# Kernel tuning notes

Hardware: AMD Instinct MI355X
Metric: run time of the kernel (lower is better)

The kernel has to match this reference:

```python
import jax, jax.numpy as jnp
import numpy as np

NUM_HEADS = 16
HEAD_DIM = 128


def apply_rope(x, rope):
    # x: [B, H, N, D]; rope: [N, 1, D]
    freqs = rope[:, 0, :]  # [N, D]
    cos = jnp.repeat(freqs[:, 0::2], 2, axis=-1)[None, None]  # [1,1,N,D]
    sin = jnp.repeat(freqs[:, 1::2], 2, axis=-1)[None, None]
    xr = x.reshape(*x.shape[:-1], -1, 2)
    x_real, x_imag = xr[..., 0], xr[..., 1]
    x_rot = jnp.stack([-x_imag, x_real], axis=-1).reshape(x.shape)
    return (x * cos + x_rot * sin).astype(x.dtype)


def setup_inputs() -> dict:
    key = jax.random.key(0)
    k1, k2, k3, k4 = jax.random.split(key, 4)
    B, N, hidden = 2, 2048, 2048
    x = jax.random.normal(k1, (B, N, hidden), dtype=jnp.float32)
    rope = jax.random.uniform(k2, (N, 1, HEAD_DIM), dtype=jnp.float32)
    qkv_w = jax.random.normal(k3, (hidden, 3 * NUM_HEADS * HEAD_DIM), dtype=jnp.float32) * 0.02
    out_w = jax.random.normal(k4, (NUM_HEADS * HEAD_DIM, hidden), dtype=jnp.float32) * 0.02
    return {"x": x, "rope": rope, "qkv_w": qkv_w, "out_w": out_w}


def reference(x, rope, qkv_w, out_w):
    B, N, _ = x.shape
    H, D = NUM_HEADS, HEAD_DIM
    qkv = (x @ qkv_w).reshape(B, N, 3, H, D)  # [B,N,3,H,D]
    q = jnp.transpose(qkv[:, :, 0], (0, 2, 1, 3))  # [B,H,N,D]
    k = jnp.transpose(qkv[:, :, 1], (0, 2, 1, 3))
    v = jnp.transpose(qkv[:, :, 2], (0, 2, 1, 3))
    q = apply_rope(q, rope)
    k = apply_rope(k, rope)
    scale = 1.0 / np.float32(np.sqrt(D))
    scores = jnp.einsum('bhqd,bhkd->bhqk', q, k) * scale
    attn = jax.nn.softmax(scores, axis=-1)
    out = jnp.einsum('bhqk,bhkd->bhqd', attn, v)
    out = jnp.transpose(out, (0, 2, 1, 3)).reshape(B, N, H * D)
    return out @ out_w
```

## Files before the change

### kernel.cpp

```cpp
#include <hip/hip_runtime.h>
#include <stdint.h>


typedef unsigned short u16;
typedef __bf16 bf16x8 __attribute__((ext_vector_type(8)));
typedef float f32x4 __attribute__((ext_vector_type(4)));

#define DI static __device__ __forceinline__

DI u16 f2b(float f) {
  union { float f; unsigned u; } v; v.f = f;
  unsigned r = v.u + 0x7FFFu + ((v.u >> 16) & 1u);
  return (u16)(r >> 16);
}

typedef unsigned int __attribute__((address_space(1))) *gas1_t;
typedef unsigned int __attribute__((address_space(3))) *las3_t;

DI void async16(const void* g, void* l) {
  __builtin_amdgcn_global_load_lds((gas1_t)g, (las3_t)l, 16, 0, 0);
}

DI bf16x8 ldsv(const u16* p) { return *(const bf16x8*)p; }

__global__ void k_cvt(const float* __restrict__ in, u16* __restrict__ out, int n4) {
  int i = blockIdx.x * blockDim.x + threadIdx.x;
  if (i >= n4) return;
  float4 v = ((const float4*)in)[i];
  ushort4 o;
  o.x = f2b(v.x); o.y = f2b(v.y); o.z = f2b(v.z); o.w = f2b(v.w);
  ((ushort4*)out)[i] = o;
}

__global__ void k_tcvt(const float* __restrict__ in, u16* __restrict__ out, int R, int C) {
  __shared__ float t[32][33];
  int bx = blockIdx.x * 32, by = blockIdx.y * 32;
  int tx = threadIdx.x, ty = threadIdx.y;
#pragma unroll
  for (int i = 0; i < 4; i++)
    t[ty + i * 8][tx] = in[(size_t)(by + ty + i * 8) * C + bx + tx];
  __syncthreads();
#pragma unroll
  for (int i = 0; i < 4; i++)
    out[(size_t)(bx + ty + i * 8) * R + by + tx] = f2b(t[tx][ty + i * 8]);
}

template <int MODE>
__global__ __launch_bounds__(256) void k_gemm(
    const u16* __restrict__ A, const u16* __restrict__ BT, const int K,
    float* __restrict__ C, const int ldc,
    const float* __restrict__ rope,
    u16* __restrict__ Qp, u16* __restrict__ Kp, u16* __restrict__ VTp) {
  __shared__ u16 As[4096];
  __shared__ u16 Bs[4096];
  const int tid = threadIdx.x;
  const int w = tid >> 6, lane = tid & 63;
  const int g = lane >> 4, lr = lane & 15;
  const int wm = (w >> 1) << 6, wn = (w & 1) << 6;
  const int bm0 = blockIdx.y << 7, bn0 = blockIdx.x << 7;

  const int cg = (lane & 3) ^ ((lane >> 3) & 3);
  const int l4 = lane >> 2;
  const int gsw = g ^ ((lr >> 1) & 3);

  const u16* Ag = A + (size_t)(bm0 + (w << 5) + l4) * K + (cg << 3);
  const u16* Bg = BT + (size_t)(bn0 + (w << 5) + l4) * K + (cg << 3);
  u16* Asd = As + (w << 10);
  u16* Bsd = Bs + (w << 10);
  const size_t rstep = (size_t)K << 4;

  const f32x4 zf = {0.f, 0.f, 0.f, 0.f};
  f32x4 acc[4][4];
#pragma unroll
  for (int i = 0; i < 4; i++)
#pragma unroll
    for (int j = 0; j < 4; j++) acc[i][j] = zf;

  for (int kt = 0; kt < K; kt += 32) {
    async16(Ag + kt, Asd);
    async16(Ag + rstep + kt, Asd + 512);
    async16(Bg + kt, Bsd);
    async16(Bg + rstep + kt, Bsd + 512);
    __syncthreads();
    bf16x8 af[4], bf[4];
#pragma unroll
    for (int i = 0; i < 4; i++) {
      af[i] = ldsv(As + ((wm + (i << 4) + lr) << 5) + (gsw << 3));
      bf[i] = ldsv(Bs + ((wn + (i << 4) + lr) << 5) + (gsw << 3));
    }
#pragma unroll
    for (int i = 0; i < 4; i++)
#pragma unroll
      for (int j = 0; j < 4; j++)
        acc[i][j] = __builtin_amdgcn_mfma_f32_16x16x32_bf16(af[i], bf[j], acc[i][j], 0, 0, 0);
    __syncthreads();
  }

  if constexpr (MODE == 0) {
#pragma unroll
    for (int i = 0; i < 4; i++) {
      const int row0 = bm0 + wm + (i << 4) + (g << 2);
#pragma unroll
      for (int j = 0; j < 4; j++) {
        const int col = bn0 + wn + (j << 4) + lr;
#pragma unroll
        for (int e = 0; e < 4; e++)
          C[(size_t)(row0 + e) * ldc + col] = acc[i][j][e];
      }
    }
  } else {
    const int sidx = bn0 >> 11;
    const int h = (bn0 >> 7) & 15;
    const int b = bm0 >> 11;
    const int nb = (bm0 & 2047) + wm;
    if (sidx < 2) {
      u16* dst = (sidx == 0 ? Qp : Kp) + ((size_t)(b * 16 + h) << 18);
      const float qs = (sidx == 0) ? 0.08838834764831845f : 1.0f;
#pragma unroll
      for (int i = 0; i < 4; i++) {
#pragma unroll
        for (int j = 0; j < 4; j++) {
          const int d = wn + (j << 4) + lr;
          const float sg = (d & 1) ? 1.f : -1.f;
          const int dpe = d & ~1, dpo = d | 1;
#pragma unroll
          for (int e = 0; e < 4; e++) {
            const int n = nb + (i << 4) + (g << 2) + e;
            const float v = acc[i][j][e];
            const float p = __shfl_xor(v, 1);
            const float cf = rope[(n << 7) + dpe];
            const float sf = rope[(n << 7) + dpo];
            dst[((size_t)n << 7) + d] = f2b((v * cf + sg * p * sf) * qs);
          }
        }
      }
    } else {
      u16* dst = VTp + ((size_t)(b * 16 + h) << 18);
#pragma unroll
      for (int i = 0; i < 4; i++) {
#pragma unroll
        for (int j = 0; j < 4; j++) {
          const int d = wn + (j << 4) + lr;
          const int n0 = nb + (i << 4) + (g << 2);
          ushort4 o;
          o.x = f2b(acc[i][j][0]); o.y = f2b(acc[i][j][1]);
          o.z = f2b(acc[i][j][2]); o.w = f2b(acc[i][j][3]);
          *(ushort4*)(dst + ((size_t)d << 11) + n0) = o;
        }
      }
    }
  }
}

__global__ __launch_bounds__(256) void k_attn(
    const u16* __restrict__ Q, const u16* __restrict__ Kt,
    const u16* __restrict__ VT, u16* __restrict__ Og) {
  __shared__ u16 KV[16384];
  __shared__ u16 Pb[4][4096];
  const int tid = threadIdx.x;
  const int w = tid >> 6, lane = tid & 63;
  const int g = lane >> 4, lr = lane & 15;
  const int qt = blockIdx.x, h = blockIdx.y, b = blockIdx.z;
  const size_t bh = (size_t)(b * 16 + h) << 18;
  const u16* Qb = Q + bh;
  const u16* Kb = Kt + bh;
  const u16* Vb = VT + bh;
  u16* Pw = &Pb[w][0];

  const int qr0 = (qt << 7) + (w << 5);
  bf16x8 qf[2][4];
#pragma unroll
  for (int mi = 0; mi < 2; mi++)
#pragma unroll
    for (int kk = 0; kk < 4; kk++)
      qf[mi][kk] = *(const bf16x8*)(Qb + ((size_t)(qr0 + (mi << 4) + lr) << 7) + (kk << 5) + (g << 3));

  const f32x4 zf = {0.f, 0.f, 0.f, 0.f};
  f32x4 o[2][8];
  float m_[2][4], l_[2][4];
#pragma unroll
  for (int mi = 0; mi < 2; mi++) {
#pragma unroll
    for (int ni = 0; ni < 8; ni++) o[mi][ni] = zf;
#pragma unroll
    for (int e = 0; e < 4; e++) { m_[mi][e] = -3.0e38f; l_[mi][e] = 0.f; }
  }

  for (int kt = 0; kt < 16; kt++) {
#pragma unroll
    for (int q = 0; q < 8; q++) {
      const int r = (((w << 3) + q) << 2) + g;
      const int cc = lr ^ (((q << 2) + g) & 7);
      async16(Kb + ((size_t)((kt << 7) + r) << 7) + (cc << 3), KV + (((w << 3) + q) << 9));
    }
    __syncthreads();
    f32x4 s[2][8];
#pragma unroll
    for (int mi = 0; mi < 2; mi++)
#pragma unroll
      for (int ni = 0; ni < 8; ni++) s[mi][ni] = zf;
#pragma unroll
    for (int kk = 0; kk < 4; kk++) {
      bf16x8 kf[8];
#pragma unroll
      for (int ni = 0; ni < 8; ni++) {
        const int row = (ni << 4) + lr;
        kf[ni] = ldsv(KV + (row << 7) + ((((kk << 2) + g) ^ (row & 7)) << 3));
      }
#pragma unroll
      for (int mi = 0; mi < 2; mi++)
#pragma unroll
        for (int ni = 0; ni < 8; ni++)
          s[mi][ni] = __builtin_amdgcn_mfma_f32_16x16x32_bf16(qf[mi][kk], kf[ni], s[mi][ni], 0, 0, 0);
    }
    __syncthreads();
#pragma unroll
    for (int q = 0; q < 8; q++) {
      const int r = (((w << 3) + q) << 2) + g;
      const int cc = lr ^ (((q << 2) + g) & 7);
      async16(Vb + ((size_t)r << 11) + (kt << 7) + (cc << 3), KV + (((w << 3) + q) << 9));
    }
#pragma unroll
    for (int mi = 0; mi < 2; mi++) {
      float mx[4], al[4], ps[4];
#pragma unroll
      for (int e = 0; e < 4; e++) {
        float v = s[mi][0][e];
#pragma unroll
        for (int ni = 1; ni < 8; ni++) v = fmaxf(v, s[mi][ni][e]);
        v = fmaxf(v, __shfl_xor(v, 1));
        v = fmaxf(v, __shfl_xor(v, 2));
        v = fmaxf(v, __shfl_xor(v, 4));
        v = fmaxf(v, __shfl_xor(v, 8));
        mx[e] = fmaxf(v, m_[mi][e]);
        al[e] = __expf(m_[mi][e] - mx[e]);
        m_[mi][e] = mx[e];
        ps[e] = 0.f;
      }
#pragma unroll
      for (int ni = 0; ni < 8; ni++)
#pragma unroll
        for (int e = 0; e < 4; e++) {
          const float p = __expf(s[mi][ni][e] - mx[e]);
          s[mi][ni][e] = p;
          ps[e] += p;
        }
#pragma unroll
      for (int e = 0; e < 4; e++) {
        ps[e] += __shfl_xor(ps[e], 1);
        ps[e] += __shfl_xor(ps[e], 2);
        ps[e] += __shfl_xor(ps[e], 4);
        ps[e] += __shfl_xor(ps[e], 8);
        l_[mi][e] = l_[mi][e] * al[e] + ps[e];
      }
#pragma unroll
      for (int ni = 0; ni < 8; ni++)
#pragma unroll
        for (int e = 0; e < 4; e++) o[mi][ni][e] *= al[e];
#pragma unroll
      for (int ni = 0; ni < 8; ni++)
#pragma unroll
        for (int e = 0; e < 4; e++) {
          const int row = (mi << 4) + (g << 2) + e;
          const int col = (ni << 4) + lr;
          Pw[(row << 7) + (((col >> 3) ^ (row & 7)) << 3) + (col & 7)] = f2b(s[mi][ni][e]);
        }
    }
    __syncthreads();
#pragma unroll
    for (int kk = 0; kk < 4; kk++) {
      bf16x8 pf[2];
#pragma unroll
      for (int mi = 0; mi < 2; mi++) {
        const int row = (mi << 4) + lr;
        pf[mi] = ldsv(Pw + (row << 7) + ((((kk << 2) + g) ^ (row & 7)) << 3));
      }
      bf16x8 vf[8];
#pragma unroll
      for (int ni = 0; ni < 8; ni++) {
        const int d = (ni << 4) + lr;
        vf[ni] = ldsv(KV + (d << 7) + ((((kk << 2) + g) ^ (d & 7)) << 3));
      }
#pragma unroll
      for (int mi = 0; mi < 2; mi++)
#pragma unroll
        for (int ni = 0; ni < 8; ni++)
          o[mi][ni] = __builtin_amdgcn_mfma_f32_16x16x32_bf16(pf[mi], vf[ni], o[mi][ni], 0, 0, 0);
    }
    __syncthreads();
  }
  u16* Ob = Og + ((size_t)b << 22) + (h << 7);
#pragma unroll
  for (int mi = 0; mi < 2; mi++) {
    float inv[4];
#pragma unroll
    for (int e = 0; e < 4; e++) inv[e] = 1.0f / l_[mi][e];
#pragma unroll
    for (int ni = 0; ni < 8; ni++) {
      const int d = (ni << 4) + lr;
#pragma unroll
      for (int e = 0; e < 4; e++) {
        const int n = qr0 + (mi << 4) + (g << 2) + e;
        Ob[((size_t)n << 11) + d] = f2b(o[mi][ni][e] * inv[e]);
      }
    }
  }
}

extern "C" void kernel_launch(void* const* d_in, const int* in_sizes, int n_in,
                              void* d_out, int out_size, void* d_ws, size_t ws_size,
                              hipStream_t stream) {
  const float* x = (const float*)d_in[0];
  const float* rope = (const float*)d_in[1];
  const float* qkv_w = (const float*)d_in[2];
  const float* out_w = (const float*)d_in[3];
  float* out = (float*)d_out;

  char* ws = (char*)d_ws;
  u16* xb    = (u16*)(ws);
  u16* wqkvT = (u16*)(ws + 16777216);
  u16* woT   = (u16*)(ws + 41943040);
  u16* Qp    = (u16*)(ws + 50331648);
  u16* Kp    = (u16*)(ws + 67108864);
  u16* VTp   = (u16*)(ws + 83886080);
  u16* Og    = xb;

  k_cvt<<<8192, 256, 0, stream>>>(x, xb, 2097152);
  k_tcvt<<<dim3(192, 64), dim3(32, 8), 0, stream>>>(qkv_w, wqkvT, 2048, 6144);
  k_tcvt<<<dim3(64, 64), dim3(32, 8), 0, stream>>>(out_w, woT, 2048, 2048);
  k_gemm<1><<<dim3(48, 32), 256, 0, stream>>>(xb, wqkvT, 2048, nullptr, 0, rope, Qp, Kp, VTp);
  k_attn<<<dim3(16, 16, 2), 256, 0, stream>>>(Qp, Kp, VTp, Og);
  k_gemm<0><<<dim3(16, 32), 256, 0, stream>>>(Og, woT, 2048, out, 2048, nullptr, nullptr, nullptr, nullptr);
}
```

Measured before the change: 514.4 us.

## Rework attention pipeline with split K/V buffers, lazy rescale, exp2, deeper GEMM k-tile

The GEMM k-step grows from 32 to 64 with an 8-way XOR swizzle, which halves the number of barrier-separated iterations. Attention now uses 64-key tiles with separate K and V LDS buffers, so the next K/V loads are issued behind the current compute. It also folds log2(e) into the Q scale so it can use exp2, skips output rescaling unless the running max grows by more than 8, adds setprio around MFMA bursts, sets launch bounds to allow 2 blocks per CU, and remaps blocks through a 1D grid. The lazy rescale trades a little numeric headroom for fewer multiplies, and the smaller tile means twice as many loop iterations.

Measured after the change: 442.0 us. 1.16x faster.

```diff
diff --git a/kernel.cpp b/kernel.cpp
--- a/kernel.cpp
+++ b/kernel.cpp
@@ -13,6 +13,12 @@
   unsigned r = v.u + 0x7FFFu + ((v.u >> 16) & 1u);
   return (u16)(r >> 16);
 }
+
+#if __has_builtin(__builtin_amdgcn_exp2f)
+DI float EXP2(float x) { return __builtin_amdgcn_exp2f(x); }
+#else
+DI float EXP2(float x) { return exp2f(x); }
+#endif
 
 typedef unsigned int __attribute__((address_space(1))) *gas1_t;
 typedef unsigned int __attribute__((address_space(3))) *las3_t;
@@ -51,23 +57,22 @@
     float* __restrict__ C, const int ldc,
     const float* __restrict__ rope,
     u16* __restrict__ Qp, u16* __restrict__ Kp, u16* __restrict__ VTp) {
-  __shared__ u16 As[4096];
-  __shared__ u16 Bs[4096];
+  __shared__ u16 As[8192];
+  __shared__ u16 Bs[8192];
   const int tid = threadIdx.x;
   const int w = tid >> 6, lane = tid & 63;
   const int g = lane >> 4, lr = lane & 15;
   const int wm = (w >> 1) << 6, wn = (w & 1) << 6;
   const int bm0 = blockIdx.y << 7, bn0 = blockIdx.x << 7;
 
-  const int cg = (lane & 3) ^ ((lane >> 3) & 3);
-  const int l4 = lane >> 2;
-  const int gsw = g ^ ((lr >> 1) & 3);
-
-  const u16* Ag = A + (size_t)(bm0 + (w << 5) + l4) * K + (cg << 3);
-  const u16* Bg = BT + (size_t)(bn0 + (w << 5) + l4) * K + (cg << 3);
-  u16* Asd = As + (w << 10);
-  u16* Bsd = Bs + (w << 10);
-  const size_t rstep = (size_t)K << 4;
+  const int cg8 = (lane & 7) ^ (lane >> 3);
+  const int row_l = lane >> 3;
+
+  const u16* Ag = A + (size_t)(bm0 + (w << 5) + row_l) * K + (cg8 << 3);
+  const u16* Bg = BT + (size_t)(bn0 + (w << 5) + row_l) * K + (cg8 << 3);
+  u16* Asd = As + (w << 11);
+  u16* Bsd = Bs + (w << 11);
+  const size_t rstep = (size_t)K << 3;
 
   const f32x4 zf = {0.f, 0.f, 0.f, 0.f};
   f32x4 acc[4][4];
@@ -76,23 +81,28 @@
 #pragma unroll
     for (int j = 0; j < 4; j++) acc[i][j] = zf;
 
-  for (int kt = 0; kt < K; kt += 32) {
-    async16(Ag + kt, Asd);
-    async16(Ag + rstep + kt, Asd + 512);
-    async16(Bg + kt, Bsd);
-    async16(Bg + rstep + kt, Bsd + 512);
+  for (int kt = 0; kt < K; kt += 64) {
+#pragma unroll
+    for (int i = 0; i < 4; i++) {
+      async16(Ag + (size_t)i * rstep + kt, Asd + (i << 9));
+      async16(Bg + (size_t)i * rstep + kt, Bsd + (i << 9));
+    }
     __syncthreads();
-    bf16x8 af[4], bf[4];
-#pragma unroll
-    for (int i = 0; i < 4; i++) {
-      af[i] = ldsv(As + ((wm + (i << 4) + lr) << 5) + (gsw << 3));
-      bf[i] = ldsv(Bs + ((wn + (i << 4) + lr) << 5) + (gsw << 3));
-    }
-#pragma unroll
-    for (int i = 0; i < 4; i++)
-#pragma unroll
-      for (int j = 0; j < 4; j++)
-        acc[i][j] = __builtin_amdgcn_mfma_f32_16x16x32_bf16(af[i], bf[j], acc[i][j], 0, 0, 0);
+#pragma unroll
+    for (int kk = 0; kk < 2; kk++) {
+      bf16x8 af[4], bf[4];
+      const int swz = ((((kk << 2) + g) ^ (lr & 7)) << 3);
+#pragma unroll
+      for (int i = 0; i < 4; i++) {
+        af[i] = ldsv(As + ((wm + (i << 4) + lr) << 6) + swz);
+        bf[i] = ldsv(Bs + ((wn + (i << 4) + lr) << 6) + swz);
+      }
+#pragma unroll
+      for (int i = 0; i < 4; i++)
+#pragma unroll
+        for (int j = 0; j < 4; j++)
+          acc[i][j] = __builtin_amdgcn_mfma_f32_16x16x32_bf16(af[i], bf[j], acc[i][j], 0, 0, 0);
+    }
     __syncthreads();
   }
 
@@ -115,7 +125,7 @@
     const int nb = (bm0 & 2047) + wm;
     if (sidx < 2) {
       u16* dst = (sidx == 0 ? Qp : Kp) + ((size_t)(b * 16 + h) << 18);
-      const float qs = (sidx == 0) ? 0.08838834764831845f : 1.0f;
+      const float qs = (sidx == 0) ? 0.08838834764831845f * 1.4426950408889634f : 1.0f;
 #pragma unroll
       for (int i = 0; i < 4; i++) {
 #pragma unroll
@@ -152,15 +162,17 @@
   }
 }
 
-__global__ __launch_bounds__(256) void k_attn(
+__global__ __launch_bounds__(256, 2) void k_attn(
     const u16* __restrict__ Q, const u16* __restrict__ Kt,
     const u16* __restrict__ VT, u16* __restrict__ Og) {
-  __shared__ u16 KV[16384];
-  __shared__ u16 Pb[4][4096];
+  __shared__ u16 Ks[8192];
+  __shared__ u16 Vs[8192];
+  __shared__ u16 Pb[4][2048];
   const int tid = threadIdx.x;
   const int w = tid >> 6, lane = tid & 63;
   const int g = lane >> 4, lr = lane & 15;
-  const int qt = blockIdx.x, h = blockIdx.y, b = blockIdx.z;
+  const int wgid = ((blockIdx.x & 7) << 6) + (blockIdx.x >> 3);
+  const int qt = wgid & 15, h = (wgid >> 4) & 15, b = wgid >> 8;
   const size_t bh = (size_t)(b * 16 + h) << 18;
   const u16* Qb = Q + bh;
   const u16* Kb = Kt + bh;
@@ -175,6 +187,30 @@
     for (int kk = 0; kk < 4; kk++)
       qf[mi][kk] = *(const bf16x8*)(Qb + ((size_t)(qr0 + (mi << 4) + lr) << 7) + (kk << 5) + (g << 3));
 
+  const int krow_l = lane >> 4;
+  const int kcg_base = lane & 15;
+  const int vrow_l = lane >> 3;
+  const int vcg_base = lane & 7;
+
+  auto stageK = [&](int kt) {
+#pragma unroll
+    for (int i = 0; i < 4; i++) {
+      const int grp = (w << 2) + i;
+      const int row = (grp << 2) + krow_l;
+      const int cg = kcg_base ^ (row & 7);
+      async16(Kb + ((size_t)((kt << 6) + row) << 7) + (cg << 3), Ks + (grp << 9));
+    }
+  };
+  auto stageV = [&](int kt) {
+#pragma unroll
+    for (int i = 0; i < 4; i++) {
+      const int grp = (w << 2) + i;
+      const int d = (grp << 3) + vrow_l;
+      const int cg = vcg_base ^ (d & 7);
+      async16(Vb + ((size_t)d << 11) + (kt << 6) + (cg << 3), Vs + (grp << 9));
+    }
+  };
+
   const f32x4 zf = {0.f, 0.f, 0.f, 0.f};
   f32x4 o[2][8];
   float m_[2][4], l_[2][4];
@@ -183,112 +219,139 @@
 #pragma unroll
     for (int ni = 0; ni < 8; ni++) o[mi][ni] = zf;
 #pragma unroll
-    for (int e = 0; e < 4; e++) { m_[mi][e] = -3.0e38f; l_[mi][e] = 0.f; }
-  }
-
-  for (int kt = 0; kt < 16; kt++) {
-#pragma unroll
-    for (int q = 0; q < 8; q++) {
-      const int r = (((w << 3) + q) << 2) + g;
-      const int cc = lr ^ (((q << 2) + g) & 7);
-      async16(Kb + ((size_t)((kt << 7) + r) << 7) + (cc << 3), KV + (((w << 3) + q) << 9));
-    }
-    __syncthreads();
-    f32x4 s[2][8];
-#pragma unroll
-    for (int mi = 0; mi < 2; mi++)
-#pragma unroll
-      for (int ni = 0; ni < 8; ni++) s[mi][ni] = zf;
+    for (int e = 0; e < 4; e++) { m_[mi][e] = -1.0e30f; l_[mi][e] = 0.f; }
+  }
+
+  stageK(0);
+  stageV(0);
+  __syncthreads();
+
+  for (int kt = 0; kt < 32; kt++) {
+    f32x4 s[2][4];
+#pragma unroll
+    for (int mi = 0; mi < 2; mi++)
+#pragma unroll
+      for (int ni = 0; ni < 4; ni++) s[mi][ni] = zf;
 #pragma unroll
     for (int kk = 0; kk < 4; kk++) {
-      bf16x8 kf[8];
-#pragma unroll
-      for (int ni = 0; ni < 8; ni++) {
+      bf16x8 kf[4];
+#pragma unroll
+      for (int ni = 0; ni < 4; ni++) {
         const int row = (ni << 4) + lr;
-        kf[ni] = ldsv(KV + (row << 7) + ((((kk << 2) + g) ^ (row & 7)) << 3));
-      }
+        kf[ni] = ldsv(Ks + (row << 7) + ((((kk << 2) + g) ^ (row & 7)) << 3));
+      }
+      __builtin_amdgcn_s_setprio(1);
 #pragma unroll
       for (int mi = 0; mi < 2; mi++)
 #pragma unroll
-        for (int ni = 0; ni < 8; ni++)
+        for (int ni = 0; ni < 4; ni++)
           s[mi][ni] = __builtin_amdgcn_mfma_f32_16x16x32_bf16(qf[mi][kk], kf[ni], s[mi][ni], 0, 0, 0);
-    }
-    __syncthreads();
-#pragma unroll
-    for (int q = 0; q < 8; q++) {
-      const int r = (((w << 3) + q) << 2) + g;
-      const int cc = lr ^ (((q << 2) + g) & 7);
-      async16(Vb + ((size_t)r << 11) + (kt << 7) + (cc << 3), KV + (((w << 3) + q) << 9));
-    }
-#pragma unroll
-    for (int mi = 0; mi < 2; mi++) {
-      float mx[4], al[4], ps[4];
+      __builtin_amdgcn_s_setprio(0);
+    }
+
+    float pm[2][4];
+#pragma unroll
+    for (int mi = 0; mi < 2; mi++)
 #pragma unroll
       for (int e = 0; e < 4; e++) {
-        float v = s[mi][0][e];
-#pragma unroll
-        for (int ni = 1; ni < 8; ni++) v = fmaxf(v, s[mi][ni][e]);
+        float v = fmaxf(fmaxf(s[mi][0][e], s[mi][1][e]), fmaxf(s[mi][2][e], s[mi][3][e]));
         v = fmaxf(v, __shfl_xor(v, 1));
         v = fmaxf(v, __shfl_xor(v, 2));
         v = fmaxf(v, __shfl_xor(v, 4));
         v = fmaxf(v, __shfl_xor(v, 8));
-        mx[e] = fmaxf(v, m_[mi][e]);
-        al[e] = __expf(m_[mi][e] - mx[e]);
-        m_[mi][e] = mx[e];
-        ps[e] = 0.f;
-      }
-#pragma unroll
-      for (int ni = 0; ni < 8; ni++)
+        pm[mi][e] = v;
+      }
+    bool need = false;
+#pragma unroll
+    for (int mi = 0; mi < 2; mi++)
+#pragma unroll
+      for (int e = 0; e < 4; e++) need = need || (pm[mi][e] > m_[mi][e] + 8.0f);
+    if (__any(need)) {
+      float al[2][4];
+#pragma unroll
+      for (int mi = 0; mi < 2; mi++)
 #pragma unroll
         for (int e = 0; e < 4; e++) {
-          const float p = __expf(s[mi][ni][e] - mx[e]);
+          const float mn = fmaxf(m_[mi][e], pm[mi][e]);
+          const float a = EXP2(m_[mi][e] - mn);
+          m_[mi][e] = mn;
+          l_[mi][e] *= a;
+          al[mi][e] = a;
+        }
+#pragma unroll
+      for (int mi = 0; mi < 2; mi++)
+#pragma unroll
+        for (int ni = 0; ni < 8; ni++)
+#pragma unroll
+          for (int e = 0; e < 4; e++) o[mi][ni][e] *= al[mi][e];
+    }
+    float ps[2][4];
+#pragma unroll
+    for (int mi = 0; mi < 2; mi++)
+#pragma unroll
+      for (int e = 0; e < 4; e++) ps[mi][e] = 0.f;
+#pragma unroll
+    for (int mi = 0; mi < 2; mi++)
+#pragma unroll
+      for (int ni = 0; ni < 4; ni++)
+#pragma unroll
+        for (int e = 0; e < 4; e++) {
+          const float p = EXP2(s[mi][ni][e] - m_[mi][e]);
           s[mi][ni][e] = p;
-          ps[e] += p;
-        }
+          ps[mi][e] += p;
+        }
+#pragma unroll
+    for (int mi = 0; mi < 2; mi++)
 #pragma unroll
       for (int e = 0; e < 4; e++) {
-        ps[e] += __shfl_xor(ps[e], 1);
-        ps[e] += __shfl_xor(ps[e], 2);
-        ps[e] += __shfl_xor(ps[e], 4);
-        ps[e] += __shfl_xor(ps[e], 8);
-        l_[mi][e] = l_[mi][e] * al[e] + ps[e];
-      }
-#pragma unroll
-      for (int ni = 0; ni < 8; ni++)
-#pragma unroll
-        for (int e = 0; e < 4; e++) o[mi][ni][e] *= al[e];
-#pragma unroll
-      for (int ni = 0; ni < 8; ni++)
+        float t = ps[mi][e];
+        t += __shfl_xor(t, 1);
+        t += __shfl_xor(t, 2);
+        t += __shfl_xor(t, 4);
+        t += __shfl_xor(t, 8);
+        l_[mi][e] += t;
+      }
+#pragma unroll
+    for (int mi = 0; mi < 2; mi++)
+#pragma unroll
+      for (int ni = 0; ni < 4; ni++)
 #pragma unroll
         for (int e = 0; e < 4; e++) {
           const int row = (mi << 4) + (g << 2) + e;
           const int col = (ni << 4) + lr;
-          Pw[(row << 7) + (((col >> 3) ^ (row & 7)) << 3) + (col & 7)] = f2b(s[mi][ni][e]);
-        }
-    }
+          Pw[(row << 6) + (((col >> 3) ^ (row & 7)) << 3) + (col & 7)] = f2b(s[mi][ni][e]);
+        }
+
     __syncthreads();
-#pragma unroll
-    for (int kk = 0; kk < 4; kk++) {
+    if (kt < 31) stageK(kt + 1);
+
+#pragma unroll
+    for (int kk = 0; kk < 2; kk++) {
       bf16x8 pf[2];
 #pragma unroll
       for (int mi = 0; mi < 2; mi++) {
         const int row = (mi << 4) + lr;
-        pf[mi] = ldsv(Pw + (row << 7) + ((((kk << 2) + g) ^ (row & 7)) << 3));
+        pf[mi] = ldsv(Pw + (row << 6) + ((((kk << 2) + g) ^ (row & 7)) << 3));
       }
       bf16x8 vf[8];
 #pragma unroll
       for (int ni = 0; ni < 8; ni++) {
         const int d = (ni << 4) + lr;
-        vf[ni] = ldsv(KV + (d << 7) + ((((kk << 2) + g) ^ (d & 7)) << 3));
-      }
+        vf[ni] = ldsv(Vs + (d << 6) + ((((kk << 2) + g) ^ (d & 7)) << 3));
+      }
+      __builtin_amdgcn_s_setprio(1);
 #pragma unroll
       for (int mi = 0; mi < 2; mi++)
 #pragma unroll
         for (int ni = 0; ni < 8; ni++)
           o[mi][ni] = __builtin_amdgcn_mfma_f32_16x16x32_bf16(pf[mi], vf[ni], o[mi][ni], 0, 0, 0);
-    }
+      __builtin_amdgcn_s_setprio(0);
+    }
+
     __syncthreads();
-  }
+    if (kt < 31) stageV(kt + 1);
+  }
+
   u16* Ob = Og + ((size_t)b << 22) + (h << 7);
 #pragma unroll
   for (int mi = 0; mi < 2; mi++) {
@@ -329,6 +392,6 @@
   k_tcvt<<<dim3(192, 64), dim3(32, 8), 0, stream>>>(qkv_w, wqkvT, 2048, 6144);
   k_tcvt<<<dim3(64, 64), dim3(32, 8), 0, stream>>>(out_w, woT, 2048, 2048);
   k_gemm<1><<<dim3(48, 32), 256, 0, stream>>>(xb, wqkvT, 2048, nullptr, 0, rope, Qp, Kp, VTp);
-  k_attn<<<dim3(16, 16, 2), 256, 0, stream>>>(Qp, Kp, VTp, Og);
+  k_attn<<<512, 256, 0, stream>>>(Qp, Kp, VTp, Og);
   k_gemm<0><<<dim3(16, 32), 256, 0, stream>>>(Og, woT, 2048, out, 2048, nullptr, nullptr, nullptr, nullptr);
 }
```
